# Kernel tuning notes

Hardware: AMD Instinct MI355X
Metric: run time of the kernel (lower is better)

Reference implementation:

```python
import jax, jax.numpy as jnp
import numpy as np

NEG = -9e15
ALPHA = 0.2  # LeakyReLU negative slope


def setup_inputs() -> dict:
    key = jax.random.key(0)
    k1, k2, k3, k4, k5, k6 = jax.random.split(key, 6)
    N, Fin, Fout = 8192, 512, 64
    x = jax.random.normal(k1, (N, Fin), dtype=jnp.float32)
    adj = jax.random.randint(k2, (N, N), 0, 2, dtype=jnp.int32)
    W = jax.random.normal(k3, (Fin, Fout), dtype=jnp.float32) * 0.05
    b = jax.random.normal(k4, (Fout,), dtype=jnp.float32) * 0.05
    a = jax.random.normal(k5, (2 * Fout,), dtype=jnp.float32) * 0.05
    a_b = jax.random.normal(k6, (), dtype=jnp.float32) * 0.05
    return {"x": x, "adj": adj, "W": W, "b": b, "a": a, "a_b": a_b}


def reference(x, adj, W, b, a, a_b):
    Fout = W.shape[1]
    h = x @ W + b  # [N, Fout]
    # attn([h_i, h_j]) decomposes: e[i,j] = h_i . a_src + h_j . a_dst + a_b
    # (avoids materializing the [N, N, 2F] concat tensor; same math)
    s_src = h @ a[:Fout]  # [N]
    s_dst = h @ a[Fout:]  # [N]
    energy = s_src[:, None] + s_dst[None, :] + a_b  # [N, N]
    energy = jnp.where(energy > 0, energy, ALPHA * energy)  # LeakyReLU
    masked = jnp.where(adj > 0, energy, NEG)
    attn = jax.nn.softmax(masked, axis=-1)  # dropout p=0 in eval
    h_prime = attn @ h  # [N, Fout]
    return jax.nn.elu(h_prime)  # concat=True path
```

## Files before the change

### kernel.cpp

```cpp
#include <hip/hip_runtime.h>
#include <hip/hip_bf16.h>

#define N_NODES 8192
#define FIN 512
#define FOUT 64
#define LRELU_ALPHA 0.2f

typedef __attribute__((ext_vector_type(8))) short short8;
typedef __attribute__((ext_vector_type(4))) float floatx4;

static __device__ __forceinline__ short f2bf_bits(float x) {
    union { __hip_bfloat16 b; short s; } u; u.b = __float2bfloat16(x); return u.s;
}

static __device__ __forceinline__ float pval(float ssrc, float sd, int adjv) {
    float e = ssrc + sd;
    e = fmaxf(e, LRELU_ALPHA * e);
    float pv = __expf(e);
    return adjv > 0 ? pv : 0.0f;
}

__global__ __launch_bounds__(256) void gat_h(
    const float* __restrict__ x, const float* __restrict__ W,
    const float* __restrict__ bias, const float* __restrict__ a,
    const float* __restrict__ a_b,
    float* __restrict__ s_src, float* __restrict__ s_dst,
    unsigned short* __restrict__ hswz)
{
    const int lane = threadIdx.x & 63;
    const int wave = threadIdx.x >> 6;
    const int r0 = (blockIdx.x * 4 + wave) * 4;

    float acc0 = 0.f, acc1 = 0.f, acc2 = 0.f, acc3 = 0.f;
    const float* x0 = x + (size_t)r0 * FIN;

    #pragma unroll 4
    for (int k = 0; k < FIN; k += 4) {
        float4 xa = *reinterpret_cast<const float4*>(x0 + k);
        float4 xb = *reinterpret_cast<const float4*>(x0 + FIN + k);
        float4 xc = *reinterpret_cast<const float4*>(x0 + 2 * FIN + k);
        float4 xd = *reinterpret_cast<const float4*>(x0 + 3 * FIN + k);
        float w0 = W[(k + 0) * FOUT + lane];
        float w1 = W[(k + 1) * FOUT + lane];
        float w2 = W[(k + 2) * FOUT + lane];
        float w3 = W[(k + 3) * FOUT + lane];
        acc0 = fmaf(xa.w, w3, fmaf(xa.z, w2, fmaf(xa.y, w1, fmaf(xa.x, w0, acc0))));
        acc1 = fmaf(xb.w, w3, fmaf(xb.z, w2, fmaf(xb.y, w1, fmaf(xb.x, w0, acc1))));
        acc2 = fmaf(xc.w, w3, fmaf(xc.z, w2, fmaf(xc.y, w1, fmaf(xc.x, w0, acc2))));
        acc3 = fmaf(xd.w, w3, fmaf(xd.z, w2, fmaf(xd.y, w1, fmaf(xd.x, w0, acc3))));
    }
    float bb = bias[lane];
    acc0 += bb; acc1 += bb; acc2 += bb; acc3 += bb;

    {
        const int ks = r0 >> 5;
        const int n = lane >> 4;
        const int lane_dst = (lane & 15) + (((r0 >> 3) & 3) << 4);
        const int e0 = r0 & 7;
        ushort4 pk;
        pk.x = (unsigned short)f2bf_bits(acc0);
        pk.y = (unsigned short)f2bf_bits(acc1);
        pk.z = (unsigned short)f2bf_bits(acc2);
        pk.w = (unsigned short)f2bf_bits(acc3);
        *reinterpret_cast<ushort4*>(
            hswz + (size_t)((ks * 4 + n) * 64 + lane_dst) * 8 + e0) = pk;
    }

    float asrc = a[lane], adst = a[FOUT + lane];
    float ab = a_b[0];
    float ss0 = acc0 * asrc, ss1 = acc1 * asrc, ss2 = acc2 * asrc, ss3 = acc3 * asrc;
    float sd0 = acc0 * adst, sd1 = acc1 * adst, sd2 = acc2 * adst, sd3 = acc3 * adst;
    #pragma unroll
    for (int m = 32; m >= 1; m >>= 1) {
        ss0 += __shfl_xor(ss0, m); ss1 += __shfl_xor(ss1, m);
        ss2 += __shfl_xor(ss2, m); ss3 += __shfl_xor(ss3, m);
        sd0 += __shfl_xor(sd0, m); sd1 += __shfl_xor(sd1, m);
        sd2 += __shfl_xor(sd2, m); sd3 += __shfl_xor(sd3, m);
    }
    if (lane == 0) {
        float4 vs = { ss0 + ab, ss1 + ab, ss2 + ab, ss3 + ab };
        float4 vd = { sd0, sd1, sd2, sd3 };
        *reinterpret_cast<float4*>(s_src + r0) = vs;
        *reinterpret_cast<float4*>(s_dst + r0) = vd;
    }
}

static __device__ __forceinline__ void stage_tile(const int* __restrict__ adj,
                                                  int i0, int j0, int lane,
                                                  char* ldsbase) {
    #pragma unroll
    for (int t = 0; t < 4; ++t) {
        const int r = t * 4 + (lane >> 4);
        const int u = (lane & 15) * 4;
        const int col = u ^ ((r & 7) << 2);
        const int* g = adj + (size_t)(i0 + r) * N_NODES + j0 + col;
        __builtin_amdgcn_global_load_lds(
            (const __attribute__((address_space(1))) int*)g,
            (__attribute__((address_space(3))) int*)(ldsbase + t * 1024),
            16, 0, 0);
    }
}

__global__ __launch_bounds__(512, 4) void gat_attn(
    const int* __restrict__ adj,
    const float* __restrict__ s_src,
    const float* __restrict__ s_dst,
    const unsigned short* __restrict__ hswz,
    float* __restrict__ out)
{
    __shared__ __align__(16) char smem[65536];

    const int lane = threadIdx.x & 63;
    const int wave = threadIdx.x >> 6;
    const int i0 = blockIdx.x * 16;
    const int rowA = i0 + (lane & 15);
    const int ko = (lane >> 4) * 8;

    const float ssrc = s_src[rowA];
    floatx4 acc[4] = { {0.f,0.f,0.f,0.f},{0.f,0.f,0.f,0.f},
                       {0.f,0.f,0.f,0.f},{0.f,0.f,0.f,0.f} };
    float denom = 0.f;

    char* buf0 = smem + wave * 8192;
    char* buf1 = buf0 + 4096;

    const int NT = (N_NODES / 64) / 8;
    int jt = wave;
    stage_tile(adj, i0, jt * 64, lane, buf0);

    for (int t = 0; t < NT; ++t) {
        const int* cur = (const int*)((t & 1) ? buf1 : buf0);
        char* nxt = (t & 1) ? buf0 : buf1;

        asm volatile("s_waitcnt vmcnt(0)" ::: "memory");
        __builtin_amdgcn_sched_barrier(0);

        if (t + 1 < NT) stage_tile(adj, i0, (jt + 8) * 64, lane, nxt);

        const int j0 = jt * 64;
        const int r = lane & 15;
        const int swz = (r & 7) << 2;
        #pragma unroll
        for (int kk = 0; kk < 2; ++kk) {
            const int c0 = kk * 32 + ko;
            int4 A0 = *reinterpret_cast<const int4*>(cur + r * 64 + (c0 ^ swz));
            int4 A1 = *reinterpret_cast<const int4*>(cur + r * 64 + ((c0 + 4) ^ swz));
            const int jb = j0 + c0;
            float4 S0 = *reinterpret_cast<const float4*>(s_dst + jb);
            float4 S1 = *reinterpret_cast<const float4*>(s_dst + jb + 4);
            float p0 = pval(ssrc, S0.x, A0.x);
            float p1 = pval(ssrc, S0.y, A0.y);
            float p2 = pval(ssrc, S0.z, A0.z);
            float p3 = pval(ssrc, S0.w, A0.w);
            float p4 = pval(ssrc, S1.x, A1.x);
            float p5 = pval(ssrc, S1.y, A1.y);
            float p6 = pval(ssrc, S1.z, A1.z);
            float p7 = pval(ssrc, S1.w, A1.w);
            denom += ((p0 + p1) + (p2 + p3)) + ((p4 + p5) + (p6 + p7));
            short8 af;
            af[0] = f2bf_bits(p0); af[1] = f2bf_bits(p1);
            af[2] = f2bf_bits(p2); af[3] = f2bf_bits(p3);
            af[4] = f2bf_bits(p4); af[5] = f2bf_bits(p5);
            af[6] = f2bf_bits(p6); af[7] = f2bf_bits(p7);
            const int ks = jt * 2 + kk;
            #pragma unroll
            for (int n = 0; n < 4; ++n) {
                short8 bf = *reinterpret_cast<const short8*>(
                    hswz + (size_t)((ks * 4 + n) * 64 + lane) * 8);
                acc[n] = __builtin_amdgcn_mfma_f32_16x16x32_bf16(af, bf, acc[n], 0, 0, 0);
            }
        }
        jt += 8;
    }

    denom += __shfl_xor(denom, 16);
    denom += __shfl_xor(denom, 32);

    __syncthreads();
    floatx4* redbuf = (floatx4*)smem;
    float* dred = (float*)(smem + 32768);
    #pragma unroll
    for (int n = 0; n < 4; ++n) redbuf[(wave * 4 + n) * 64 + lane] = acc[n];
    if (lane < 16) dred[wave * 16 + lane] = denom;
    __syncthreads();

    if (wave < 4) {
        floatx4 facc = redbuf[wave * 64 + lane];
        #pragma unroll
        for (int v = 1; v < 8; ++v) facc += redbuf[(v * 4 + wave) * 64 + lane];
        #pragma unroll
        for (int e = 0; e < 4; ++e) {
            const int r2 = (lane >> 4) * 4 + e;
            float dn = 0.f;
            #pragma unroll
            for (int v = 0; v < 8; ++v) dn += dred[v * 16 + r2];
            float val = facc[e] / dn;
            val = val > 0.f ? val : (__expf(val) - 1.f);
            out[(size_t)(i0 + r2) * FOUT + wave * 16 + (lane & 15)] = val;
        }
    }
}

extern "C" void kernel_launch(void* const* d_in, const int* in_sizes, int n_in,
                              void* d_out, int out_size, void* d_ws, size_t ws_size,
                              hipStream_t stream) {
    const float* x   = (const float*)d_in[0];
    const int*   adj = (const int*)d_in[1];
    const float* W   = (const float*)d_in[2];
    const float* b   = (const float*)d_in[3];
    const float* a   = (const float*)d_in[4];
    const float* a_b = (const float*)d_in[5];
    float* out = (float*)d_out;

    char* ws = (char*)d_ws;
    float* s_src = (float*)ws;
    float* s_dst = (float*)(ws + 32 * 1024);
    unsigned short* hswz = (unsigned short*)(ws + 64 * 1024);

    hipLaunchKernelGGL(gat_h, dim3(N_NODES / 16), dim3(256), 0, stream,
                       x, W, b, a, a_b, s_src, s_dst, hswz);
    hipLaunchKernelGGL(gat_attn, dim3(N_NODES / 16), dim3(512), 0, stream,
                       adj, s_src, s_dst, hswz, out);
}
```

Before: 132.1 us.

## Stage block-wide adj slabs with full-row loads and widen h projection per wave

The attention kernel now stages a 16x512 adjacency slab per step, shared by the whole block. Each wave loads two full contiguous 2KB rows instead of each wave fetching its own 16x64 tile, so global reads of adj become long row-contiguous runs. The double buffer uses 64KB of LDS, with a __syncthreads per slab instead of a per-wave vmcnt wait, and the occupancy hint on launch bounds is dropped. The h projection kernel computes 8 rows per wave and writes full short8 packs, halving the grid and reusing each W load across more rows.

```diff
diff --git a/kernel.cpp b/kernel.cpp
--- a/kernel.cpp
+++ b/kernel.cpp
@@ -5,6 +5,8 @@
 #define FIN 512
 #define FOUT 64
 #define LRELU_ALPHA 0.2f
+#define SLAB 512
+#define NSLAB (N_NODES / SLAB)
 
 typedef __attribute__((ext_vector_type(8))) short short8;
 typedef __attribute__((ext_vector_type(4))) float floatx4;
@@ -29,79 +31,63 @@
 {
     const int lane = threadIdx.x & 63;
     const int wave = threadIdx.x >> 6;
-    const int r0 = (blockIdx.x * 4 + wave) * 4;
-
-    float acc0 = 0.f, acc1 = 0.f, acc2 = 0.f, acc3 = 0.f;
+    const int r0 = (blockIdx.x * 4 + wave) * 8;
+
+    float acc[8] = {0.f,0.f,0.f,0.f,0.f,0.f,0.f,0.f};
     const float* x0 = x + (size_t)r0 * FIN;
 
-    #pragma unroll 4
+    #pragma unroll 2
     for (int k = 0; k < FIN; k += 4) {
-        float4 xa = *reinterpret_cast<const float4*>(x0 + k);
-        float4 xb = *reinterpret_cast<const float4*>(x0 + FIN + k);
-        float4 xc = *reinterpret_cast<const float4*>(x0 + 2 * FIN + k);
-        float4 xd = *reinterpret_cast<const float4*>(x0 + 3 * FIN + k);
         float w0 = W[(k + 0) * FOUT + lane];
         float w1 = W[(k + 1) * FOUT + lane];
         float w2 = W[(k + 2) * FOUT + lane];
         float w3 = W[(k + 3) * FOUT + lane];
-        acc0 = fmaf(xa.w, w3, fmaf(xa.z, w2, fmaf(xa.y, w1, fmaf(xa.x, w0, acc0))));
-        acc1 = fmaf(xb.w, w3, fmaf(xb.z, w2, fmaf(xb.y, w1, fmaf(xb.x, w0, acc1))));
-        acc2 = fmaf(xc.w, w3, fmaf(xc.z, w2, fmaf(xc.y, w1, fmaf(xc.x, w0, acc2))));
-        acc3 = fmaf(xd.w, w3, fmaf(xd.z, w2, fmaf(xd.y, w1, fmaf(xd.x, w0, acc3))));
+        #pragma unroll
+        for (int rr = 0; rr < 8; ++rr) {
+            float4 xv = *reinterpret_cast<const float4*>(x0 + (size_t)rr * FIN + k);
+            acc[rr] = fmaf(xv.w, w3, fmaf(xv.z, w2, fmaf(xv.y, w1, fmaf(xv.x, w0, acc[rr]))));
+        }
     }
     float bb = bias[lane];
-    acc0 += bb; acc1 += bb; acc2 += bb; acc3 += bb;
+    #pragma unroll
+    for (int rr = 0; rr < 8; ++rr) acc[rr] += bb;
 
     {
         const int ks = r0 >> 5;
         const int n = lane >> 4;
         const int lane_dst = (lane & 15) + (((r0 >> 3) & 3) << 4);
-        const int e0 = r0 & 7;
-        ushort4 pk;
-        pk.x = (unsigned short)f2bf_bits(acc0);
-        pk.y = (unsigned short)f2bf_bits(acc1);
-        pk.z = (unsigned short)f2bf_bits(acc2);
-        pk.w = (unsigned short)f2bf_bits(acc3);
-        *reinterpret_cast<ushort4*>(
-            hswz + (size_t)((ks * 4 + n) * 64 + lane_dst) * 8 + e0) = pk;
+        short8 pk;
+        #pragma unroll
+        for (int rr = 0; rr < 8; ++rr) pk[rr] = f2bf_bits(acc[rr]);
+        *reinterpret_cast<short8*>(hswz + (size_t)((ks * 4 + n) * 64 + lane_dst) * 8) = pk;
     }
 
     float asrc = a[lane], adst = a[FOUT + lane];
     float ab = a_b[0];
-    float ss0 = acc0 * asrc, ss1 = acc1 * asrc, ss2 = acc2 * asrc, ss3 = acc3 * asrc;
-    float sd0 = acc0 * adst, sd1 = acc1 * adst, sd2 = acc2 * adst, sd3 = acc3 * adst;
+    float ss[8], sd[8];
+    #pragma unroll
+    for (int rr = 0; rr < 8; ++rr) { ss[rr] = acc[rr] * asrc; sd[rr] = acc[rr] * adst; }
     #pragma unroll
     for (int m = 32; m >= 1; m >>= 1) {
-        ss0 += __shfl_xor(ss0, m); ss1 += __shfl_xor(ss1, m);
-        ss2 += __shfl_xor(ss2, m); ss3 += __shfl_xor(ss3, m);
-        sd0 += __shfl_xor(sd0, m); sd1 += __shfl_xor(sd1, m);
-        sd2 += __shfl_xor(sd2, m); sd3 += __shfl_xor(sd3, m);
+        #pragma unroll
+        for (int rr = 0; rr < 8; ++rr) {
+            ss[rr] += __shfl_xor(ss[rr], m);
+            sd[rr] += __shfl_xor(sd[rr], m);
+        }
     }
     if (lane == 0) {
-        float4 vs = { ss0 + ab, ss1 + ab, ss2 + ab, ss3 + ab };
-        float4 vd = { sd0, sd1, sd2, sd3 };
-        *reinterpret_cast<float4*>(s_src + r0) = vs;
-        *reinterpret_cast<float4*>(s_dst + r0) = vd;
-    }
-}
-
-static __device__ __forceinline__ void stage_tile(const int* __restrict__ adj,
-                                                  int i0, int j0, int lane,
-                                                  char* ldsbase) {
-    #pragma unroll
-    for (int t = 0; t < 4; ++t) {
-        const int r = t * 4 + (lane >> 4);
-        const int u = (lane & 15) * 4;
-        const int col = u ^ ((r & 7) << 2);
-        const int* g = adj + (size_t)(i0 + r) * N_NODES + j0 + col;
-        __builtin_amdgcn_global_load_lds(
-            (const __attribute__((address_space(1))) int*)g,
-            (__attribute__((address_space(3))) int*)(ldsbase + t * 1024),
-            16, 0, 0);
-    }
-}
-
-__global__ __launch_bounds__(512, 4) void gat_attn(
+        float4 v0 = { ss[0] + ab, ss[1] + ab, ss[2] + ab, ss[3] + ab };
+        float4 v1 = { ss[4] + ab, ss[5] + ab, ss[6] + ab, ss[7] + ab };
+        float4 u0 = { sd[0], sd[1], sd[2], sd[3] };
+        float4 u1 = { sd[4], sd[5], sd[6], sd[7] };
+        *reinterpret_cast<float4*>(s_src + r0)     = v0;
+        *reinterpret_cast<float4*>(s_src + r0 + 4) = v1;
+        *reinterpret_cast<float4*>(s_dst + r0)     = u0;
+        *reinterpret_cast<float4*>(s_dst + r0 + 4) = u1;
+    }
+}
+
+__global__ __launch_bounds__(512) void gat_attn(
     const int* __restrict__ adj,
     const float* __restrict__ s_src,
     const float* __restrict__ s_dst,
@@ -113,39 +99,50 @@
     const int lane = threadIdx.x & 63;
     const int wave = threadIdx.x >> 6;
     const int i0 = blockIdx.x * 16;
-    const int rowA = i0 + (lane & 15);
+    const int r = lane & 15;
     const int ko = (lane >> 4) * 8;
 
-    const float ssrc = s_src[rowA];
+    const float ssrc = s_src[i0 + r];
     floatx4 acc[4] = { {0.f,0.f,0.f,0.f},{0.f,0.f,0.f,0.f},
                        {0.f,0.f,0.f,0.f},{0.f,0.f,0.f,0.f} };
     float denom = 0.f;
 
-    char* buf0 = smem + wave * 8192;
-    char* buf1 = buf0 + 4096;
-
-    const int NT = (N_NODES / 64) / 8;
-    int jt = wave;
-    stage_tile(adj, i0, jt * 64, lane, buf0);
-
-    for (int t = 0; t < NT; ++t) {
-        const int* cur = (const int*)((t & 1) ? buf1 : buf0);
-        char* nxt = (t & 1) ? buf0 : buf1;
-
-        asm volatile("s_waitcnt vmcnt(0)" ::: "memory");
-        __builtin_amdgcn_sched_barrier(0);
-
-        if (t + 1 < NT) stage_tile(adj, i0, (jt + 8) * 64, lane, nxt);
-
-        const int j0 = jt * 64;
-        const int r = lane & 15;
-        const int swz = (r & 7) << 2;
+    char* buf0 = smem;
+    char* buf1 = smem + 32768;
+
+    auto stage = [&](char* buf, int s) {
+        #pragma unroll
+        for (int q = 0; q < 4; ++q) {
+            const int row = wave * 2 + (q >> 1);
+            const int half = q & 1;
+            const int* g = adj + (size_t)(i0 + row) * N_NODES + s * SLAB
+                         + half * 256 + ((lane ^ (row & 7)) << 2);
+            __builtin_amdgcn_global_load_lds(
+                (const __attribute__((address_space(1))) int*)g,
+                (__attribute__((address_space(3))) int*)(buf + row * 2048 + half * 1024),
+                16, 0, 0);
+        }
+    };
+
+    stage(buf0, 0);
+    __syncthreads();
+
+    for (int s = 0; s < NSLAB; ++s) {
+        const char* cur = (s & 1) ? buf1 : buf0;
+        char* nxt = (s & 1) ? buf0 : buf1;
+        if (s + 1 < NSLAB) stage(nxt, s + 1);
+
+        const int rbase = r * 2048;
         #pragma unroll
         for (int kk = 0; kk < 2; ++kk) {
-            const int c0 = kk * 32 + ko;
-            int4 A0 = *reinterpret_cast<const int4*>(cur + r * 64 + (c0 ^ swz));
-            int4 A1 = *reinterpret_cast<const int4*>(cur + r * 64 + ((c0 + 4) ^ swz));
-            const int jb = j0 + c0;
+            const int c0 = wave * 64 + kk * 32 + ko;
+            const int hb = (c0 >> 8) << 10;
+            const int c = c0 & 255;
+            const int g0 = (((c >> 2) + 0) ^ (r & 7)) << 4;
+            const int g1 = (((c >> 2) + 1) ^ (r & 7)) << 4;
+            int4 A0 = *reinterpret_cast<const int4*>(cur + rbase + hb + g0);
+            int4 A1 = *reinterpret_cast<const int4*>(cur + rbase + hb + g1);
+            const int jb = s * SLAB + c0;
             float4 S0 = *reinterpret_cast<const float4*>(s_dst + jb);
             float4 S1 = *reinterpret_cast<const float4*>(s_dst + jb + 4);
             float p0 = pval(ssrc, S0.x, A0.x);
@@ -162,7 +159,7 @@
             af[2] = f2bf_bits(p2); af[3] = f2bf_bits(p3);
             af[4] = f2bf_bits(p4); af[5] = f2bf_bits(p5);
             af[6] = f2bf_bits(p6); af[7] = f2bf_bits(p7);
-            const int ks = jt * 2 + kk;
+            const int ks = (jb >> 5);
             #pragma unroll
             for (int n = 0; n < 4; ++n) {
                 short8 bf = *reinterpret_cast<const short8*>(
@@ -170,13 +167,12 @@
                 acc[n] = __builtin_amdgcn_mfma_f32_16x16x32_bf16(af, bf, acc[n], 0, 0, 0);
             }
         }
-        jt += 8;
+        __syncthreads();
     }
 
     denom += __shfl_xor(denom, 16);
     denom += __shfl_xor(denom, 32);
 
-    __syncthreads();
     floatx4* redbuf = (floatx4*)smem;
     float* dred = (float*)(smem + 32768);
     #pragma unroll
@@ -217,7 +213,7 @@
     float* s_dst = (float*)(ws + 32 * 1024);
     unsigned short* hswz = (unsigned short*)(ws + 64 * 1024);
 
-    hipLaunchKernelGGL(gat_h, dim3(N_NODES / 16), dim3(256), 0, stream,
+    hipLaunchKernelGGL(gat_h, dim3(N_NODES / 32), dim3(256), 0, stream,
                        x, W, b, a, a_b, s_src, s_dst, hswz);
     hipLaunchKernelGGL(gat_attn, dim3(N_NODES / 16), dim3(512), 0, stream,
                        adj, s_src, s_dst, hswz, out);
```

Result: slower. 136.2 us (+3.2%).

## Pack adjacency into bitmask in separate kernel and stage x through LDS

Applied to the files above, without the earlier changes.

A new kernel compresses the int32 adjacency matrix into 64-bit ballot bitmasks. The attention kernel then loads each block's 16 rows of mask bits into LDS once and tests individual bits, where it used to stream int32 adjacency tiles through double-buffered LDS. The projection kernel also stages x tiles in LDS with async global-to-LDS loads. The adjacency still has to be read in full once by the new pass, so the gain depends on the attention kernel no longer being bound by adjacency bandwidth, and the extra launch plus the bitmask write are added costs.

```diff
diff --git a/kernel.cpp b/kernel.cpp
--- a/kernel.cpp
+++ b/kernel.cpp
@@ -13,13 +13,22 @@
     union { __hip_bfloat16 b; short s; } u; u.b = __float2bfloat16(x); return u.s;
 }
 
-static __device__ __forceinline__ float pval(float ssrc, float sd, int adjv) {
-    float e = ssrc + sd;
-    e = fmaxf(e, LRELU_ALPHA * e);
-    float pv = __expf(e);
-    return adjv > 0 ? pv : 0.0f;
-}
-
+__global__ __launch_bounds__(256) void adj_bits(
+    const int* __restrict__ adj, unsigned long long* __restrict__ bits)
+{
+    const int lane = threadIdx.x & 63;
+    const int wid = blockIdx.x * 4 + (threadIdx.x >> 6);
+    const size_t base = (size_t)wid * 128;
+    const int* src = adj + base * 64 + lane;
+    #pragma unroll 8
+    for (int t = 0; t < 128; ++t) {
+        int v = src[t * 64];
+        unsigned long long m = __ballot(v > 0);
+        if (lane == 0) bits[base + t] = m;
+    }
+}
+
+#define GH_KT 128
 __global__ __launch_bounds__(256) void gat_h(
     const float* __restrict__ x, const float* __restrict__ W,
     const float* __restrict__ bias, const float* __restrict__ a,
@@ -27,28 +36,52 @@
     float* __restrict__ s_src, float* __restrict__ s_dst,
     unsigned short* __restrict__ hswz)
 {
+    __shared__ __align__(16) float xlds[2][16][GH_KT];
+
     const int lane = threadIdx.x & 63;
     const int wave = threadIdx.x >> 6;
-    const int r0 = (blockIdx.x * 4 + wave) * 4;
+    const int i0 = blockIdx.x * 16;
+    const int r0 = i0 + wave * 4;
+
+    auto stage = [&](int buf, int k0) {
+        #pragma unroll
+        for (int d = 0; d < 2; ++d) {
+            const int row = wave * 4 + d * 2 + (lane >> 5);
+            const float* g = x + (size_t)(i0 + row) * FIN + k0 + (lane & 31) * 4;
+            __builtin_amdgcn_global_load_lds(
+                (const __attribute__((address_space(1))) float*)g,
+                (__attribute__((address_space(3))) float*)&xlds[buf][wave * 4 + d * 2][0],
+                16, 0, 0);
+        }
+    };
 
     float acc0 = 0.f, acc1 = 0.f, acc2 = 0.f, acc3 = 0.f;
-    const float* x0 = x + (size_t)r0 * FIN;
-
-    #pragma unroll 4
-    for (int k = 0; k < FIN; k += 4) {
-        float4 xa = *reinterpret_cast<const float4*>(x0 + k);
-        float4 xb = *reinterpret_cast<const float4*>(x0 + FIN + k);
-        float4 xc = *reinterpret_cast<const float4*>(x0 + 2 * FIN + k);
-        float4 xd = *reinterpret_cast<const float4*>(x0 + 3 * FIN + k);
-        float w0 = W[(k + 0) * FOUT + lane];
-        float w1 = W[(k + 1) * FOUT + lane];
-        float w2 = W[(k + 2) * FOUT + lane];
-        float w3 = W[(k + 3) * FOUT + lane];
-        acc0 = fmaf(xa.w, w3, fmaf(xa.z, w2, fmaf(xa.y, w1, fmaf(xa.x, w0, acc0))));
-        acc1 = fmaf(xb.w, w3, fmaf(xb.z, w2, fmaf(xb.y, w1, fmaf(xb.x, w0, acc1))));
-        acc2 = fmaf(xc.w, w3, fmaf(xc.z, w2, fmaf(xc.y, w1, fmaf(xc.x, w0, acc2))));
-        acc3 = fmaf(xd.w, w3, fmaf(xd.z, w2, fmaf(xd.y, w1, fmaf(xd.x, w0, acc3))));
-    }
+
+    stage(0, 0);
+    for (int kt = 0; kt < FIN / GH_KT; ++kt) {
+        asm volatile("s_waitcnt vmcnt(0)" ::: "memory");
+        __builtin_amdgcn_sched_barrier(0);
+        if (kt + 1 < FIN / GH_KT) stage((kt + 1) & 1, (kt + 1) * GH_KT);
+
+        const float* xt = &xlds[kt & 1][wave * 4][0];
+        const int k0 = kt * GH_KT;
+        #pragma unroll 4
+        for (int k4 = 0; k4 < GH_KT / 4; ++k4) {
+            float w0 = W[(k0 + k4 * 4 + 0) * FOUT + lane];
+            float w1 = W[(k0 + k4 * 4 + 1) * FOUT + lane];
+            float w2 = W[(k0 + k4 * 4 + 2) * FOUT + lane];
+            float w3 = W[(k0 + k4 * 4 + 3) * FOUT + lane];
+            float4 xa = *reinterpret_cast<const float4*>(xt + 0 * GH_KT + k4 * 4);
+            float4 xb = *reinterpret_cast<const float4*>(xt + 1 * GH_KT + k4 * 4);
+            float4 xc = *reinterpret_cast<const float4*>(xt + 2 * GH_KT + k4 * 4);
+            float4 xd = *reinterpret_cast<const float4*>(xt + 3 * GH_KT + k4 * 4);
+            acc0 = fmaf(xa.w, w3, fmaf(xa.z, w2, fmaf(xa.y, w1, fmaf(xa.x, w0, acc0))));
+            acc1 = fmaf(xb.w, w3, fmaf(xb.z, w2, fmaf(xb.y, w1, fmaf(xb.x, w0, acc1))));
+            acc2 = fmaf(xc.w, w3, fmaf(xc.z, w2, fmaf(xc.y, w1, fmaf(xc.x, w0, acc2))));
+            acc3 = fmaf(xd.w, w3, fmaf(xd.z, w2, fmaf(xd.y, w1, fmaf(xd.x, w0, acc3))));
+        }
+    }
+
     float bb = bias[lane];
     acc0 += bb; acc1 += bb; acc2 += bb; acc3 += bb;
 
@@ -85,84 +118,66 @@
     }
 }
 
-static __device__ __forceinline__ void stage_tile(const int* __restrict__ adj,
-                                                  int i0, int j0, int lane,
-                                                  char* ldsbase) {
-    #pragma unroll
-    for (int t = 0; t < 4; ++t) {
-        const int r = t * 4 + (lane >> 4);
-        const int u = (lane & 15) * 4;
-        const int col = u ^ ((r & 7) << 2);
-        const int* g = adj + (size_t)(i0 + r) * N_NODES + j0 + col;
-        __builtin_amdgcn_global_load_lds(
-            (const __attribute__((address_space(1))) int*)g,
-            (__attribute__((address_space(3))) int*)(ldsbase + t * 1024),
-            16, 0, 0);
-    }
-}
-
-__global__ __launch_bounds__(512, 4) void gat_attn(
-    const int* __restrict__ adj,
+__global__ __launch_bounds__(512) void gat_attn(
+    const unsigned int* __restrict__ bits,
     const float* __restrict__ s_src,
     const float* __restrict__ s_dst,
     const unsigned short* __restrict__ hswz,
     float* __restrict__ out)
 {
-    __shared__ __align__(16) char smem[65536];
+    __shared__ __align__(16) char smem[33280];
 
     const int lane = threadIdx.x & 63;
     const int wave = threadIdx.x >> 6;
     const int i0 = blockIdx.x * 16;
-    const int rowA = i0 + (lane & 15);
-    const int ko = (lane >> 4) * 8;
-
-    const float ssrc = s_src[rowA];
+    const int r = lane & 15;
+    const int g = lane >> 4;
+
+    #pragma unroll
+    for (int i = 0; i < 2; ++i) {
+        const int c = threadIdx.x + i * 512;
+        const int row = c >> 6, col = c & 63;
+        uint4 v = *reinterpret_cast<const uint4*>(bits + (size_t)(i0 + row) * 256 + col * 4);
+        *reinterpret_cast<uint4*>(smem + row * 1040 + col * 16) = v;
+    }
+    __syncthreads();
+
+    const float ssrc = s_src[i0 + r];
     floatx4 acc[4] = { {0.f,0.f,0.f,0.f},{0.f,0.f,0.f,0.f},
                        {0.f,0.f,0.f,0.f},{0.f,0.f,0.f,0.f} };
     float denom = 0.f;
 
-    char* buf0 = smem + wave * 8192;
-    char* buf1 = buf0 + 4096;
-
-    const int NT = (N_NODES / 64) / 8;
-    int jt = wave;
-    stage_tile(adj, i0, jt * 64, lane, buf0);
-
-    for (int t = 0; t < NT; ++t) {
-        const int* cur = (const int*)((t & 1) ? buf1 : buf0);
-        char* nxt = (t & 1) ? buf0 : buf1;
-
-        asm volatile("s_waitcnt vmcnt(0)" ::: "memory");
-        __builtin_amdgcn_sched_barrier(0);
-
-        if (t + 1 < NT) stage_tile(adj, i0, (jt + 8) * 64, lane, nxt);
-
-        const int j0 = jt * 64;
-        const int r = lane & 15;
-        const int swz = (r & 7) << 2;
+    const char* bl = smem + r * 1040 + (wave << 3);
+
+    for (int s = 0; s < 16; ++s) {
+        uint2 bw = *reinterpret_cast<const uint2*>(bl + s * 64);
         #pragma unroll
         for (int kk = 0; kk < 2; ++kk) {
-            const int c0 = kk * 32 + ko;
-            int4 A0 = *reinterpret_cast<const int4*>(cur + r * 64 + (c0 ^ swz));
-            int4 A1 = *reinterpret_cast<const int4*>(cur + r * 64 + ((c0 + 4) ^ swz));
-            const int jb = j0 + c0;
+            const unsigned byte = ((kk ? bw.y : bw.x) >> (g * 8)) & 0xffu;
+            const int jb = s * 512 + wave * 64 + kk * 32 + g * 8;
             float4 S0 = *reinterpret_cast<const float4*>(s_dst + jb);
             float4 S1 = *reinterpret_cast<const float4*>(s_dst + jb + 4);
-            float p0 = pval(ssrc, S0.x, A0.x);
-            float p1 = pval(ssrc, S0.y, A0.y);
-            float p2 = pval(ssrc, S0.z, A0.z);
-            float p3 = pval(ssrc, S0.w, A0.w);
-            float p4 = pval(ssrc, S1.x, A1.x);
-            float p5 = pval(ssrc, S1.y, A1.y);
-            float p6 = pval(ssrc, S1.z, A1.z);
-            float p7 = pval(ssrc, S1.w, A1.w);
+            float e0 = ssrc + S0.x, e1 = ssrc + S0.y, e2 = ssrc + S0.z, e3 = ssrc + S0.w;
+            float e4 = ssrc + S1.x, e5 = ssrc + S1.y, e6 = ssrc + S1.z, e7 = ssrc + S1.w;
+            e0 = fmaxf(e0, LRELU_ALPHA * e0); e1 = fmaxf(e1, LRELU_ALPHA * e1);
+            e2 = fmaxf(e2, LRELU_ALPHA * e2); e3 = fmaxf(e3, LRELU_ALPHA * e3);
+            e4 = fmaxf(e4, LRELU_ALPHA * e4); e5 = fmaxf(e5, LRELU_ALPHA * e5);
+            e6 = fmaxf(e6, LRELU_ALPHA * e6); e7 = fmaxf(e7, LRELU_ALPHA * e7);
+            float p0 = (byte & 1u)   ? __expf(e0) : 0.f;
+            float p1 = (byte & 2u)   ? __expf(e1) : 0.f;
+            float p2 = (byte & 4u)   ? __expf(e2) : 0.f;
+            float p3 = (byte & 8u)   ? __expf(e3) : 0.f;
+            float p4 = (byte & 16u)  ? __expf(e4) : 0.f;
+            float p5 = (byte & 32u)  ? __expf(e5) : 0.f;
+            float p6 = (byte & 64u)  ? __expf(e6) : 0.f;
+            float p7 = (byte & 128u) ? __expf(e7) : 0.f;
             denom += ((p0 + p1) + (p2 + p3)) + ((p4 + p5) + (p6 + p7));
             short8 af;
             af[0] = f2bf_bits(p0); af[1] = f2bf_bits(p1);
             af[2] = f2bf_bits(p2); af[3] = f2bf_bits(p3);
             af[4] = f2bf_bits(p4); af[5] = f2bf_bits(p5);
             af[6] = f2bf_bits(p6); af[7] = f2bf_bits(p7);
-            const int ks = jt * 2 + kk;
+            const int ks = s * 16 + wave * 2 + kk;
             #pragma unroll
             for (int n = 0; n < 4; ++n) {
                 short8 bf = *reinterpret_cast<const short8*>(
@@ -170,7 +185,6 @@
                 acc[n] = __builtin_amdgcn_mfma_f32_16x16x32_bf16(af, bf, acc[n], 0, 0, 0);
             }
         }
-        jt += 8;
     }
 
     denom += __shfl_xor(denom, 16);
@@ -216,9 +230,12 @@
     float* s_src = (float*)ws;
     float* s_dst = (float*)(ws + 32 * 1024);
     unsigned short* hswz = (unsigned short*)(ws + 64 * 1024);
-
+    unsigned long long* bitsW = (unsigned long long*)(ws + 64 * 1024 + 1024 * 1024);
+    const unsigned int* bitsR = (const unsigned int*)bitsW;
+
+    hipLaunchKernelGGL(adj_bits, dim3(N_NODES / 4), dim3(256), 0, stream, adj, bitsW);
     hipLaunchKernelGGL(gat_h, dim3(N_NODES / 16), dim3(256), 0, stream,
                        x, W, b, a, a_b, s_src, s_dst, hswz);
     hipLaunchKernelGGL(gat_attn, dim3(N_NODES / 16), dim3(512), 0, stream,
-                       adj, s_src, s_dst, hswz, out);
-}
+                       bitsR, s_src, s_dst, hswz, out);
+}
```

Result: slower. 164.2 us (+24.3%).
